# Kernel tuning notes

Hardware: AMD Instinct MI355X
Metric: run time of the kernel (lower is better)

The kernel has to match this reference:

```python
import jax, jax.numpy as jnp
import numpy as np

# Device / mapping constants (from iterator config in the original repo)
V_REF = 0.25
K_V = 2.0 * V_REF
G_MIN = 1e-5
G_MAX = 1e-3
N_AVG = 2.99
N_STD = 0.37
N_IN, N_OUT, BATCH = 1024, 512, 128


def setup_inputs() -> dict:
    key = jax.random.key(0)
    ks = jax.random.split(key, 6)
    x = jax.random.uniform(ks[0], (BATCH, N_IN), dtype=jnp.float32)
    stdv = 1.0 / np.sqrt(N_IN)
    w_pos = 0.5 + stdv * jax.random.normal(ks[1], (N_IN, N_OUT), dtype=jnp.float32)
    w_neg = 0.5 + stdv * jax.random.normal(ks[2], (N_IN, N_OUT), dtype=jnp.float32)
    b_pos = 0.5 * jnp.ones((N_OUT,), jnp.float32)
    b_neg = 0.5 * jnp.ones((N_OUT,), jnp.float32)
    # per-crosspoint I-V nonlinearity parameter n (n=2 means ohmic); clip below at 2
    n_devices = jnp.maximum(
        N_AVG + N_STD * jax.random.normal(ks[3], (N_IN + 1, 2 * N_OUT), dtype=jnp.float32),
        2.0,
    )
    return {"x": x, "w_pos": w_pos, "w_neg": w_neg, "b_pos": b_pos,
            "b_neg": b_neg, "n_devices": n_devices}


def reference(x, w_pos, w_neg, b_pos, b_neg, n_devices):
    B = x.shape[0]
    # append bias input of 1s -> [B, n_in+1]
    inputs = jnp.concatenate([x, jnp.ones((B, 1), x.dtype)], axis=1)
    # combined weights with bias row -> [n_in+1, n_out] each
    cw_pos = jnp.concatenate([w_pos, b_pos[None, :]], axis=0)
    cw_neg = jnp.concatenate([w_neg, b_neg[None, :]], axis=0)
    # interleave pos/neg columns -> [n_in+1, 2*n_out]
    combined = jnp.stack([cw_pos, cw_neg], axis=-1).reshape(cw_pos.shape[0], -1)
    # x -> V mapping
    V = K_V * inputs  # [B, n_in+1]
    # weight params -> conductances
    max_weight = jnp.max(jnp.abs(combined))
    k_G = (G_MAX - G_MIN) / max_weight
    G = k_G * jnp.abs(combined) + G_MIN  # [n_in+1, 2*n_out]
    # nonlinear I-V: I(V) = sign(V) * G*V_ref * (|V|/V_ref)^log2(n)
    exponent = jnp.log2(n_devices)          # [n_in+1, 2*n_out]
    sgn = jnp.sign(V)                       # [B, n_in+1]
    ratio = jnp.abs(V) / V_REF              # [B, n_in+1]
    I_ind = (sgn[:, :, None] * (G * V_REF)[None, :, :]
             * ratio[:, :, None] ** exponent[None, :, :])  # [B, n_in+1, 2*n_out]
    I = jnp.sum(I_ind, axis=1)              # [B, 2*n_out] (sum along bit lines)
    # differential pair currents -> output
    I_total = I[:, 0::2] - I[:, 1::2]       # [B, n_out]
    y = I_total / (K_V * k_G)
    return y
```

## Files before the change

### kernel.cpp

```cpp
#include <hip/hip_runtime.h>
#include <cstdint>
#include <cstddef>


#define B128 128
#define NIN  1024
#define NI   1025
#define NO   512
#define NJ   1024
#define SPLITS 65
#define CHUNK  16

__device__ __forceinline__ float flog2(float x) { return __builtin_amdgcn_logf(x); }
__device__ __forceinline__ float fexp2(float x) { return __builtin_amdgcn_exp2f(x); }

__global__ __launch_bounds__(1024) void k_prep(
    const float* __restrict__ x,
    const float* __restrict__ wp, const float* __restrict__ wn,
    const float* __restrict__ bp, const float* __restrict__ bn,
    float* __restrict__ LT, float* __restrict__ bmax, float* __restrict__ out)
{
    int tid = blockIdx.x * 1024 + threadIdx.x;

    out[tid] = 0.0f;

    for (int t = tid; t < NI * B128; t += 65536) {
        int i = t >> 7, b = t & 127;
        float xv = (i < NIN) ? x[b * NIN + i] : 1.0f;
        LT[t] = 1.0f + flog2(xv);
    }

    float m = 0.0f;
    for (int t = tid; t < NIN * NO; t += 65536) {
        m = fmaxf(m, fmaxf(__builtin_fabsf(wp[t]), __builtin_fabsf(wn[t])));
    }
    if (tid < NO) m = fmaxf(m, fmaxf(__builtin_fabsf(bp[tid]), __builtin_fabsf(bn[tid])));

    __shared__ float red[16];
    #pragma unroll
    for (int off = 32; off > 0; off >>= 1) m = fmaxf(m, __shfl_down(m, off, 64));
    if ((threadIdx.x & 63) == 0) red[threadIdx.x >> 6] = m;
    __syncthreads();
    if (threadIdx.x < 16) {
        m = red[threadIdx.x];
        #pragma unroll
        for (int off = 8; off > 0; off >>= 1) m = fmaxf(m, __shfl_down(m, off, 16));
        if (threadIdx.x == 0) bmax[blockIdx.x] = m;
    }
}

__global__ __launch_bounds__(512) void k_main(
    const float* __restrict__ nd,
    const float* __restrict__ wp, const float* __restrict__ wn,
    const float* __restrict__ bp, const float* __restrict__ bn,
    const float* __restrict__ LT, const float* __restrict__ bmax,
    float* __restrict__ out)
{
    const int lane = threadIdx.x & 63;

    float m = bmax[lane];
    #pragma unroll
    for (int off = 32; off > 0; off >>= 1) m = fmaxf(m, __shfl_down(m, off, 64));
    const float maxw = __shfl(m, 0, 64);
    const float kG = (1.0e-3f - 1.0e-5f) / maxw;
    const float C  = 0.5f * maxw / (1.0e-3f - 1.0e-5f);

    const int wvid = threadIdx.x >> 6;
    const int b0 = __builtin_amdgcn_readfirstlane(wvid << 4);
    const int o = (blockIdx.x << 6) + lane;
    const int i0 = blockIdx.y * CHUNK;
    int i1 = i0 + CHUNK; if (i1 > NI) i1 = NI;

    float accp[16], accn[16];
    #pragma unroll
    for (int k = 0; k < 16; ++k) { accp[k] = 0.0f; accn[k] = 0.0f; }

    for (int i = i0; i < i1; ++i) {
        const float2 nv = *(const float2*)(nd + (size_t)i * NJ + 2 * o);
        const float wvp = (i < NIN) ? wp[i * NO + o] : bp[o];
        const float wvn = (i < NIN) ? wn[i * NO + o] : bn[o];
        const float Ep = flog2(nv.x);
        const float En = flog2(nv.y);
        const float Wp = flog2(__builtin_fmaf(kG, __builtin_fabsf(wvp), 1.0e-5f));
        const float Wn = flog2(__builtin_fmaf(kG, __builtin_fabsf(wvn), 1.0e-5f));
        const float* Lrow = LT + i * B128 + b0;
        #pragma unroll
        for (int bb = 0; bb < 16; ++bb) {
            const float L = Lrow[bb];
            accp[bb] += fexp2(__builtin_fmaf(Ep, L, Wp));
            accn[bb] += fexp2(__builtin_fmaf(En, L, Wn));
        }
    }

    #pragma unroll
    for (int bb = 0; bb < 16; ++bb) {
        atomicAdd(out + (size_t)(b0 + bb) * NO + o, C * (accp[bb] - accn[bb]));
    }
}

extern "C" void kernel_launch(void* const* d_in, const int* in_sizes, int n_in,
                              void* d_out, int out_size, void* d_ws, size_t ws_size,
                              hipStream_t stream)
{
    const float* x  = (const float*)d_in[0];
    const float* wp = (const float*)d_in[1];
    const float* wn = (const float*)d_in[2];
    const float* bp = (const float*)d_in[3];
    const float* bn = (const float*)d_in[4];
    const float* nd = (const float*)d_in[5];
    float* out = (float*)d_out;

    unsigned char* ws = (unsigned char*)d_ws;
    float* bmax = (float*)ws;
    float* LT   = (float*)(ws + 256);

    k_prep<<<64, 1024, 0, stream>>>(x, wp, wn, bp, bn, LT, bmax, out);
    k_main<<<dim3(8, SPLITS), 512, 0, stream>>>(nd, wp, wn, bp, bn, LT, bmax, out);
}
```

Before: 99.97 us.

## Widen prep grid, halve main splits, prefetch next row and use unsafe atomics

The prep kernel now runs on 256 blocks, each thread handling at most one element, so the strided loops go away. The main kernel uses 32 splits of 33 rows instead of 65 of 16, which halves the number of atomic partial sums. Each iteration prefetches the next row's n/w values and preloads the 16 L values as a register software pipeline. Atomics switch to unsafeAtomicAdd, meant to use hardware float atomics. The cost is fewer blocks (256 vs 520) and so less parallelism across CUs, plus higher register pressure.

```diff
diff --git a/kernel.cpp b/kernel.cpp
--- a/kernel.cpp
+++ b/kernel.cpp
@@ -8,8 +8,10 @@
 #define NI   1025
 #define NO   512
 #define NJ   1024
-#define SPLITS 65
-#define CHUNK  16
+#define SPLITS 32
+#define CHUNK  33
+#define GMIN 1.0e-5f
+#define GSPAN (1.0e-3f - 1.0e-5f)
 
 __device__ __forceinline__ float flog2(float x) { return __builtin_amdgcn_logf(x); }
 __device__ __forceinline__ float fexp2(float x) { return __builtin_amdgcn_exp2f(x); }
@@ -20,20 +22,19 @@
     const float* __restrict__ bp, const float* __restrict__ bn,
     float* __restrict__ LT, float* __restrict__ bmax, float* __restrict__ out)
 {
-    int tid = blockIdx.x * 1024 + threadIdx.x;
+    const int tid = blockIdx.x * 1024 + threadIdx.x;
 
-    out[tid] = 0.0f;
+    if (tid < B128 * NO) out[tid] = 0.0f;
 
-    for (int t = tid; t < NI * B128; t += 65536) {
-        int i = t >> 7, b = t & 127;
+    if (tid < NI * B128) {
+        int i = tid >> 7, b = tid & 127;
         float xv = (i < NIN) ? x[b * NIN + i] : 1.0f;
-        LT[t] = 1.0f + flog2(xv);
+        LT[tid] = 1.0f + flog2(xv);
     }
 
-    float m = 0.0f;
-    for (int t = tid; t < NIN * NO; t += 65536) {
-        m = fmaxf(m, fmaxf(__builtin_fabsf(wp[t]), __builtin_fabsf(wn[t])));
-    }
+    float m0 = fmaxf(__builtin_fabsf(wp[tid]), __builtin_fabsf(wn[tid]));
+    float m1 = fmaxf(__builtin_fabsf(wp[tid + 262144]), __builtin_fabsf(wn[tid + 262144]));
+    float m = fmaxf(m0, m1);
     if (tid < NO) m = fmaxf(m, fmaxf(__builtin_fabsf(bp[tid]), __builtin_fabsf(bn[tid])));
 
     __shared__ float red[16];
@@ -58,12 +59,13 @@
 {
     const int lane = threadIdx.x & 63;
 
-    float m = bmax[lane];
+    float m = fmaxf(fmaxf(bmax[lane], bmax[lane + 64]),
+                    fmaxf(bmax[lane + 128], bmax[lane + 192]));
     #pragma unroll
     for (int off = 32; off > 0; off >>= 1) m = fmaxf(m, __shfl_down(m, off, 64));
     const float maxw = __shfl(m, 0, 64);
-    const float kG = (1.0e-3f - 1.0e-5f) / maxw;
-    const float C  = 0.5f * maxw / (1.0e-3f - 1.0e-5f);
+    const float kG = GSPAN / maxw;
+    const float C  = 0.5f * maxw / GSPAN;
 
     const int wvid = threadIdx.x >> 6;
     const int b0 = __builtin_amdgcn_readfirstlane(wvid << 4);
@@ -71,30 +73,48 @@
     const int i0 = blockIdx.y * CHUNK;
     int i1 = i0 + CHUNK; if (i1 > NI) i1 = NI;
 
-    float accp[16], accn[16];
+    float2 acc[16];
     #pragma unroll
-    for (int k = 0; k < 16; ++k) { accp[k] = 0.0f; accn[k] = 0.0f; }
+    for (int k = 0; k < 16; ++k) acc[k] = make_float2(0.0f, 0.0f);
+
+    float2 nv = *(const float2*)(nd + (size_t)i0 * NJ + 2 * o);
+    float wvp = (i0 < NIN) ? wp[i0 * NO + o] : bp[o];
+    float wvn = (i0 < NIN) ? wn[i0 * NO + o] : bn[o];
 
     for (int i = i0; i < i1; ++i) {
-        const float2 nv = *(const float2*)(nd + (size_t)i * NJ + 2 * o);
-        const float wvp = (i < NIN) ? wp[i * NO + o] : bp[o];
-        const float wvn = (i < NIN) ? wn[i * NO + o] : bn[o];
+        const int ip = (i + 1 < i1) ? i + 1 : i;
+        float2 nv_n = *(const float2*)(nd + (size_t)ip * NJ + 2 * o);
+        float wp_n = (ip < NIN) ? wp[ip * NO + o] : bp[o];
+        float wn_n = (ip < NIN) ? wn[ip * NO + o] : bn[o];
+
+        const float* Lrow = LT + i * B128 + b0;
+        float Lv[16];
+        #pragma unroll
+        for (int bb = 0; bb < 16; ++bb) Lv[bb] = Lrow[bb];
+
         const float Ep = flog2(nv.x);
         const float En = flog2(nv.y);
-        const float Wp = flog2(__builtin_fmaf(kG, __builtin_fabsf(wvp), 1.0e-5f));
-        const float Wn = flog2(__builtin_fmaf(kG, __builtin_fabsf(wvn), 1.0e-5f));
-        const float* Lrow = LT + i * B128 + b0;
+        const float Wp = flog2(__builtin_fmaf(kG, __builtin_fabsf(wvp), GMIN));
+        const float Wn = flog2(__builtin_fmaf(kG, __builtin_fabsf(wvn), GMIN));
+
         #pragma unroll
         for (int bb = 0; bb < 16; ++bb) {
-            const float L = Lrow[bb];
-            accp[bb] += fexp2(__builtin_fmaf(Ep, L, Wp));
-            accn[bb] += fexp2(__builtin_fmaf(En, L, Wn));
+            const float L = Lv[bb];
+            float ex, en;
+            ex = __builtin_fmaf(Ep, L, Wp);
+            en = __builtin_fmaf(En, L, Wn);
+            ex = fexp2(ex);
+            en = fexp2(en);
+            acc[bb].x += ex;
+            acc[bb].y += en;
         }
+
+        nv = nv_n; wvp = wp_n; wvn = wn_n;
     }
 
     #pragma unroll
     for (int bb = 0; bb < 16; ++bb) {
-        atomicAdd(out + (size_t)(b0 + bb) * NO + o, C * (accp[bb] - accn[bb]));
+        unsafeAtomicAdd(out + (size_t)(b0 + bb) * NO + o, C * (acc[bb].x - acc[bb].y));
     }
 }
 
@@ -112,8 +132,8 @@
 
     unsigned char* ws = (unsigned char*)d_ws;
     float* bmax = (float*)ws;
-    float* LT   = (float*)(ws + 256);
+    float* LT   = (float*)(ws + 4096);
 
-    k_prep<<<64, 1024, 0, stream>>>(x, wp, wn, bp, bn, LT, bmax, out);
+    k_prep<<<256, 1024, 0, stream>>>(x, wp, wn, bp, bn, LT, bmax, out);
     k_main<<<dim3(8, SPLITS), 512, 0, stream>>>(nd, wp, wn, bp, bn, LT, bmax, out);
 }
```

After: 97.33 us. -2.6%, faster.
